# Performance work log

Measured on AMD Instinct MI355X. Metric: run time of the kernel, lower is better.

The kernel has to match this reference:

```python
import jax, jax.numpy as jnp
from jax import lax
import numpy as np

V, E, H, L, B, ML, T = 32000, 512, 512, 2, 64, 64, 32


def setup_inputs() -> dict:
    key = jax.random.key(0)
    ks = jax.random.split(key, 16)
    s = 0.05
    return {
        "current_input": jax.random.randint(ks[0], (B,), 0, V),
        "h0": jax.random.normal(ks[1], (L, B, H), jnp.float32),
        "c0": jax.random.normal(ks[2], (L, B, H), jnp.float32),
        "encoder_output": jax.random.normal(ks[3], (ML, B, H), jnp.float32),
        "gtruth": jax.random.randint(ks[4], (T, B), 0, V),
        "length": T,
        "emb": s * jax.random.normal(ks[5], (V, E), jnp.float32),
        "attn_W": s * jax.random.normal(ks[6], (ML, E + H), jnp.float32),
        "attn_out_W": s * jax.random.normal(ks[7], (E, E + H), jnp.float32),
        "lstm_Wi": s * jax.random.normal(ks[8], (L, 4 * H, E), jnp.float32),
        "lstm_Wh": s * jax.random.normal(ks[9], (L, 4 * H, H), jnp.float32),
        "lstm_bi": s * jax.random.normal(ks[10], (L, 4 * H), jnp.float32),
        "lstm_bh": s * jax.random.normal(ks[11], (L, 4 * H), jnp.float32),
        "gen_W": s * jax.random.normal(ks[12], (V, H), jnp.float32),
        "gen_b": s * jax.random.normal(ks[13], (V,), jnp.float32),
    }


def _lstm_cell(x, h, c, Wi, Wh, bi, bh):
    # PyTorch gate order: i, f, g, o
    g = x @ Wi.T + h @ Wh.T + bi + bh  # [B, 4H]
    i, f, gg, o = jnp.split(g, 4, axis=-1)
    c_new = jax.nn.sigmoid(f) * c + jax.nn.sigmoid(i) * jnp.tanh(gg)
    h_new = jax.nn.sigmoid(o) * jnp.tanh(c_new)
    return h_new, c_new


def reference(current_input, h0, c0, encoder_output, gtruth, length,
              emb, attn_W, attn_out_W, lstm_Wi, lstm_Wh, lstm_bi, lstm_bh,
              gen_W, gen_b):
    n_layers = h0.shape[0]

    def step_fn(carry, tok):
        h, c = carry  # each [L, B, H]
        emb_t = emb[tok]                                   # [B, E]
        attn_in = jnp.concatenate([emb_t, h[-1]], axis=1)  # [B, E+H]
        a = jax.nn.softmax(attn_in @ attn_W.T, axis=1)     # [B, ML]
        ctx = jnp.einsum('bl,lbh->bh', a, encoder_output)  # [B, H]
        rnn_in = jax.nn.relu(
            jnp.concatenate([emb_t, ctx], axis=1) @ attn_out_W.T)  # [B, E]
        x = rnn_in
        hs, cs = [], []
        for l in range(n_layers):
            hn, cn = _lstm_cell(x, h[l], c[l], lstm_Wi[l], lstm_Wh[l],
                                lstm_bi[l], lstm_bh[l])
            hs.append(hn)
            cs.append(cn)
            x = hn
        scores = x @ gen_W.T + gen_b  # [B, V]
        return (jnp.stack(hs), jnp.stack(cs)), scores

    # teacher forcing: step t consumes current_input at t=0, gtruth[t-1] after
    tokens = jnp.concatenate([current_input[None], gtruth[:-1]], axis=0)  # [T, B]
    (h_fin, c_fin), outputs = lax.scan(step_fn, (h0, c0), tokens)
    return outputs, h_fin, c_fin
```

## Files before the change

### kernel.cpp

```cpp
#include <hip/hip_runtime.h>
#include <hip/hip_bf16.h>

typedef __bf16 bf16_t;
typedef bf16_t bf16x8 __attribute__((ext_vector_type(8)));
typedef bf16_t bf16x4 __attribute__((ext_vector_type(4)));
typedef float f32x4 __attribute__((ext_vector_type(4)));

#define MFMA(a, b, c) __builtin_amdgcn_mfma_f32_16x16x32_bf16((a), (b), (c), 0, 0, 0)

__device__ __forceinline__ float sigm(float x) { return 1.f / (1.f + __expf(-x)); }
__device__ __forceinline__ float tanh_f(float x) { return 1.f - 2.f / (__expf(2.f * x) + 1.f); }

__device__ __forceinline__ bf16x8 cvt8(const float* p) {
    f32x4 a = *(const f32x4*)p, b = *(const f32x4*)(p + 4);
    bf16x8 v;
#pragma unroll
    for (int i = 0; i < 4; ++i) { v[i] = (bf16_t)a[i]; v[4 + i] = (bf16_t)b[i]; }
    return v;
}

__device__ __forceinline__ void st4c(bf16_t* p, bf16x4 v) {
    __hip_atomic_store((unsigned long long*)p, __builtin_bit_cast(unsigned long long, v),
                       __ATOMIC_RELAXED, __HIP_MEMORY_SCOPE_AGENT);
}
__device__ __forceinline__ void st1c(bf16_t* p, bf16_t v) {
    __hip_atomic_store((unsigned short*)p, __builtin_bit_cast(unsigned short, v),
                       __ATOMIC_RELAXED, __HIP_MEMORY_SCOPE_AGENT);
}

__device__ __forceinline__ void gbar(int* cnt, int target) {
    __syncthreads();
    if (threadIdx.x == 0) {
        __hip_atomic_fetch_add(cnt, 1, __ATOMIC_RELAXED, __HIP_MEMORY_SCOPE_AGENT);
        while (__hip_atomic_load(cnt, __ATOMIC_RELAXED, __HIP_MEMORY_SCOPE_AGENT) < target)
            __builtin_amdgcn_s_sleep(2);
    }
    __syncthreads();
}

__global__ void k_cvt(const float* __restrict__ src, bf16_t* __restrict__ dst, int n) {
    int i = (blockIdx.x * 256 + threadIdx.x) * 8;
    if (i < n) *(bf16x8*)(dst + i) = cvt8(src + i);
}

__global__ void k_init(const float* __restrict__ h0, const float* __restrict__ c0,
                       const float* __restrict__ bi, const float* __restrict__ bh,
                       float* __restrict__ c_f32, bf16_t* __restrict__ h1_0,
                       bf16_t* __restrict__ h2_0, float* __restrict__ bsum,
                       int* __restrict__ bar) {
    int idx = blockIdx.x * 256 + threadIdx.x;
    if (idx < 65536) c_f32[idx] = c0[idx];
    if (idx < 32768) { h1_0[idx] = (bf16_t)h0[idx]; h2_0[idx] = (bf16_t)h0[32768 + idx]; }
    if (idx < 4096) bsum[idx] = bi[idx] + bh[idx];
    if (idx == 0) *bar = 0;
}

__global__ __launch_bounds__(256) void k_pre(const float* __restrict__ emb,
                                             const int* __restrict__ cur, const int* __restrict__ gt,
                                             const bf16_t* __restrict__ Bm, int ldb, int koff,
                                             float* __restrict__ out, int ldo) {
    int tid = threadIdx.x, lane = tid & 63, w = tid >> 6;
    int m = lane & 15, q = lane >> 4;
    int mrow = blockIdx.x * 64 + w * 16 + m;
    int tok = (mrow < 64) ? cur[mrow] : gt[mrow - 64];
    const float* arow = emb + (size_t)tok * 512;
    int n0 = blockIdx.y * 64;
    const bf16_t* brow0 = Bm + (size_t)(n0 + m) * ldb + koff;
    f32x4 acc[4] = {};
    for (int ks = 0; ks < 16; ++ks) {
        int kc = ks * 32 + q * 8;
        bf16x8 a = cvt8(arow + kc);
#pragma unroll
        for (int nt = 0; nt < 4; ++nt) {
            bf16x8 b = *(const bf16x8*)(brow0 + (size_t)nt * 16 * ldb + kc);
            acc[nt] = MFMA(a, b, acc[nt]);
        }
    }
    int rbase = blockIdx.x * 64 + w * 16 + q * 4;
#pragma unroll
    for (int nt = 0; nt < 4; ++nt)
#pragma unroll
        for (int i = 0; i < 4; ++i)
            out[(size_t)(rbase + i) * ldo + n0 + nt * 16 + m] = acc[nt][i];
}

__device__ __forceinline__ void lstm_phase(int wg, int tid,
                                           const bf16_t* __restrict__ x,
                                           const bf16_t* __restrict__ hprev,
                                           const bf16_t* __restrict__ Wi,
                                           const bf16_t* __restrict__ Wh,
                                           const float* __restrict__ bsum,
                                           float* __restrict__ c,
                                           bf16_t* __restrict__ hout,
                                           bf16_t* __restrict__ xs_out) {
    int lane = tid & 63, w = tid >> 6;
    int m = lane & 15, q = lane >> 4;
    int j0 = wg * 16;
    const bf16_t* ax = x + (size_t)(w * 16 + m) * 512;
    const bf16_t* ah = hprev + (size_t)(w * 16 + m) * 512;
    f32x4 acc[4] = {};
    for (int ks = 0; ks < 16; ++ks) {
        int kc = ks * 32 + q * 8;
        bf16x8 a = *(const bf16x8*)(ax + kc);
#pragma unroll
        for (int g = 0; g < 4; ++g) {
            const bf16_t* bp = Wi + (size_t)(g * 512 + j0 + m) * 512 + kc;
            acc[g] = MFMA(a, *(const bf16x8*)bp, acc[g]);
        }
    }
    for (int ks = 0; ks < 16; ++ks) {
        int kc = ks * 32 + q * 8;
        bf16x8 a = *(const bf16x8*)(ah + kc);
#pragma unroll
        for (int g = 0; g < 4; ++g) {
            const bf16_t* bp = Wh + (size_t)(g * 512 + j0 + m) * 512 + kc;
            acc[g] = MFMA(a, *(const bf16x8*)bp, acc[g]);
        }
    }
    int j = j0 + m;
    float bs0 = bsum[j], bs1 = bsum[512 + j], bs2 = bsum[1024 + j], bs3 = bsum[1536 + j];
#pragma unroll
    for (int i = 0; i < 4; ++i) {
        int b = w * 16 + q * 4 + i;
        float ig = acc[0][i] + bs0;
        float fg = acc[1][i] + bs1;
        float gg = acc[2][i] + bs2;
        float og = acc[3][i] + bs3;
        size_t off = (size_t)b * 512 + j;
        float co = c[off];
        float cn = sigm(fg) * co + sigm(ig) * tanh_f(gg);
        float hn = sigm(og) * tanh_f(cn);
        c[off] = cn;
        st1c(hout + off, (bf16_t)hn);
        if (xs_out) xs_out[off] = (bf16_t)hn;
    }
}

__global__ __launch_bounds__(256) void k_loop(const bf16_t* __restrict__ attn_W_bf,
                                              const bf16_t* __restrict__ attn_out_W_bf,
                                              const float* __restrict__ enc,
                                              const float* __restrict__ pre_s,
                                              const float* __restrict__ pre_r,
                                              const bf16_t* __restrict__ Wi_bf,
                                              const bf16_t* __restrict__ Wh_bf,
                                              const float* __restrict__ bsum,
                                              float* __restrict__ c_f32,
                                              bf16_t* __restrict__ h1_buf,
                                              bf16_t* __restrict__ h2_buf,
                                              bf16_t* __restrict__ ctx_buf,
                                              bf16_t* __restrict__ rnn_buf,
                                              bf16_t* __restrict__ xs,
                                              int* __restrict__ bar) {
    __shared__ float s_p[2][64];
    int tid = threadIdx.x, lane = tid & 63, w = tid >> 6;
    int m = lane & 15, q = lane >> 4;
    int wg = blockIdx.x;
    int b0 = wg * 2;
    int bt = 0;

    for (int t = 0; t < 32; ++t) {
        const bf16_t* h1p = h1_buf + (size_t)t * 32768;
        const bf16_t* h2p = h2_buf + (size_t)t * 32768;
        bf16_t* h1n = h1_buf + (size_t)(t + 1) * 32768;
        bf16_t* h2n = h2_buf + (size_t)(t + 1) * 32768;
        bf16_t* ctx_t = ctx_buf + (size_t)t * 32768;
        const bf16_t* rnn_t = rnn_buf + (size_t)t * 32768;

        {
            const bf16_t* aptr = h2p + (size_t)(b0 + (m & 1)) * 512;
            const bf16_t* bptr = attn_W_bf + (size_t)(w * 16 + m) * 1024 + 512;
            f32x4 acc = {};
            for (int ks = 0; ks < 16; ++ks) {
                int kc = ks * 32 + q * 8;
                acc = MFMA(*(const bf16x8*)(aptr + kc), *(const bf16x8*)(bptr + kc), acc);
            }
            if (q == 0) {
#pragma unroll
                for (int i = 0; i < 2; ++i)
                    s_p[i][w * 16 + m] =
                        acc[i] + pre_s[((size_t)t * 64 + b0 + i) * 64 + w * 16 + m];
            }
        }
        __syncthreads();
        if (tid < 128) {
            int r = tid >> 6, l = tid & 63;
            float v = s_p[r][l];
            float mx = v;
#pragma unroll
            for (int off = 32; off; off >>= 1) mx = fmaxf(mx, __shfl_xor(mx, off));
            float e = __expf(v - mx);
            float s = e;
#pragma unroll
            for (int off = 32; off; off >>= 1) s += __shfl_xor(s, off);
            s_p[r][l] = e / s;
        }
        __syncthreads();
        {
            int r = tid >> 7, c0 = (tid & 127) * 4;
            int b = b0 + r;
            f32x4 acc = {};
            const float* ebase = enc + (size_t)b * 512 + c0;
            for (int l = 0; l < 64; ++l) {
                float a = s_p[r][l];
                f32x4 e = *(const f32x4*)(ebase + (size_t)l * 32768);
#pragma unroll
                for (int i = 0; i < 4; ++i) acc[i] += a * e[i];
            }
            bf16x4 cv;
#pragma unroll
            for (int i = 0; i < 4; ++i) cv[i] = (bf16_t)acc[i];
            st4c(ctx_t + (size_t)b * 512 + c0, cv);
        }
        bt += 32; gbar(bar, bt);

        {
            int j0 = wg * 16;
            const bf16_t* actx = ctx_t + (size_t)(w * 16 + m) * 512;
            const bf16_t* bptr = attn_out_W_bf + (size_t)(j0 + m) * 1024 + 512;
            f32x4 acc = {};
            for (int ks = 0; ks < 16; ++ks) {
                int kc = ks * 32 + q * 8;
                acc = MFMA(*(const bf16x8*)(actx + kc), *(const bf16x8*)(bptr + kc), acc);
            }
            int jj = j0 + m;
#pragma unroll
            for (int i = 0; i < 4; ++i) {
                int b = w * 16 + q * 4 + i;
                float v = acc[i] + pre_r[((size_t)t * 64 + b) * 512 + jj];
                st1c((bf16_t*)rnn_t + (size_t)b * 512 + jj, (bf16_t)fmaxf(v, 0.f));
            }
        }
        bt += 32; gbar(bar, bt);

        lstm_phase(wg, tid, rnn_t, h1p, Wi_bf, Wh_bf, bsum, c_f32, h1n, nullptr);
        bt += 32; gbar(bar, bt);

        lstm_phase(wg, tid, h1n, h2p, Wi_bf + 1048576, Wh_bf + 1048576, bsum + 2048,
                   c_f32 + 32768, h2n, xs + (size_t)t * 32768);
        bt += 32; gbar(bar, bt);
    }
}

__global__ __launch_bounds__(256) void k_gen(const bf16_t* __restrict__ xs,
                                             const bf16_t* __restrict__ gen_W,
                                             const float* __restrict__ gen_b,
                                             float* __restrict__ out) {
    __shared__ bf16_t sA[64 * 256];
    int tid = threadIdx.x, lane = tid & 63, w = tid >> 6;
    int m = lane & 15, q4 = lane >> 4;
    int m0 = blockIdx.x * 64, n0 = blockIdx.y * 256;
    f32x4 acc[4][4] = {};
    for (int ko = 0; ko < 2; ++ko) {
        __syncthreads();
#pragma unroll
        for (int it = 0; it < 8; ++it) {
            int idx = it * 256 + tid;
            int mr = idx >> 5, qc = idx & 31;
            bf16x8 v = *(const bf16x8*)(xs + (size_t)(m0 + mr) * 512 + ko * 256 + qc * 8);
            *(bf16x8*)(&sA[(mr * 32 + (qc ^ (mr & 7))) * 8]) = v;
        }
        __syncthreads();
        const bf16_t* bbase = gen_W + (size_t)(n0 + w * 64 + m) * 512 + ko * 256;
        for (int ks = 0; ks < 8; ++ks) {
            bf16x8 af[4];
#pragma unroll
            for (int mt = 0; mt < 4; ++mt) {
                int r = mt * 16 + m, chunk = ks * 4 + q4;
                af[mt] = *(const bf16x8*)(&sA[(r * 32 + (chunk ^ (r & 7))) * 8]);
            }
            int kc = ks * 32 + q4 * 8;
#pragma unroll
            for (int nt = 0; nt < 4; ++nt) {
                bf16x8 bfrag = *(const bf16x8*)(bbase + (size_t)nt * 16 * 512 + kc);
#pragma unroll
                for (int mt = 0; mt < 4; ++mt) acc[mt][nt] = MFMA(af[mt], bfrag, acc[mt][nt]);
            }
        }
    }
#pragma unroll
    for (int nt = 0; nt < 4; ++nt) {
        int col = n0 + w * 64 + nt * 16 + m;
        float bias = gen_b[col];
#pragma unroll
        for (int mt = 0; mt < 4; ++mt)
#pragma unroll
            for (int i = 0; i < 4; ++i) {
                int r = m0 + mt * 16 + q4 * 4 + i;
                out[(size_t)r * 32000 + col] = acc[mt][nt][i] + bias;
            }
    }
}

__global__ void k_tail(const bf16_t* __restrict__ h1f, const bf16_t* __restrict__ h2f,
                       const float* __restrict__ c_f32, float* __restrict__ out) {
    int idx = blockIdx.x * 256 + threadIdx.x;
    if (idx < 65536) {
        float hv = (idx < 32768) ? (float)h1f[idx] : (float)h2f[idx - 32768];
        out[65536000 + idx] = hv;
        out[65601536 + idx] = c_f32[idx];
    }
}

extern "C" void kernel_launch(void* const* d_in, const int* in_sizes, int n_in,
                              void* d_out, int out_size, void* d_ws, size_t ws_size,
                              hipStream_t stream) {
    const int* cur = (const int*)d_in[0];
    const float* h0 = (const float*)d_in[1];
    const float* c0 = (const float*)d_in[2];
    const float* enc = (const float*)d_in[3];
    const int* gt = (const int*)d_in[4];
    const float* emb = (const float*)d_in[6];
    const float* attn_W = (const float*)d_in[7];
    const float* attn_out_W = (const float*)d_in[8];
    const float* Wi = (const float*)d_in[9];
    const float* Wh = (const float*)d_in[10];
    const float* bi = (const float*)d_in[11];
    const float* bh = (const float*)d_in[12];
    const float* gen_W = (const float*)d_in[13];
    const float* gen_b = (const float*)d_in[14];
    float* out = (float*)d_out;

    char* ws = (char*)d_ws;
    float* c_f32 = (float*)(ws + 0);
    float* bsum = (float*)(ws + 524288);
    float* pre_s = (float*)(ws + 540672);
    float* pre_r = (float*)(ws + 1064960);
    bf16_t* xs = (bf16_t*)(ws + 5324800);
    bf16_t* attn_W_bf = (bf16_t*)(ws + 7421952);
    bf16_t* attn_out_W_bf = (bf16_t*)(ws + 7553024);
    bf16_t* Wi_bf = (bf16_t*)(ws + 8601600);
    bf16_t* Wh_bf = (bf16_t*)(ws + 12795904);
    bf16_t* gen_W_bf = (bf16_t*)(ws + 16990208);
    bf16_t* h1_buf = (bf16_t*)(ws + 49758208);
    bf16_t* h2_buf = (bf16_t*)(ws + 51920896);
    bf16_t* ctx_buf = (bf16_t*)(ws + 54083584);
    bf16_t* rnn_buf = (bf16_t*)(ws + 56180736);
    int* bar = (int*)(ws + 58277888);

    k_cvt<<<32, 256, 0, stream>>>(attn_W, attn_W_bf, 65536);
    k_cvt<<<256, 256, 0, stream>>>(attn_out_W, attn_out_W_bf, 524288);
    k_cvt<<<1024, 256, 0, stream>>>(Wi, Wi_bf, 2097152);
    k_cvt<<<1024, 256, 0, stream>>>(Wh, Wh_bf, 2097152);
    k_cvt<<<8000, 256, 0, stream>>>(gen_W, gen_W_bf, 16384000);
    k_init<<<256, 256, 0, stream>>>(h0, c0, bi, bh, c_f32, h1_buf, h2_buf, bsum, bar);
    k_pre<<<dim3(32, 1), 256, 0, stream>>>(emb, cur, gt, attn_W_bf, 1024, 0, pre_s, 64);
    k_pre<<<dim3(32, 8), 256, 0, stream>>>(emb, cur, gt, attn_out_W_bf, 1024, 0, pre_r, 512);

    k_loop<<<32, 256, 0, stream>>>(attn_W_bf, attn_out_W_bf, enc, pre_s, pre_r,
                                   Wi_bf, Wh_bf, bsum, c_f32, h1_buf, h2_buf,
                                   ctx_buf, rnn_buf, xs, bar);

    k_gen<<<dim3(32, 125), 256, 0, stream>>>(xs, gen_W_bf, gen_b, out);
    k_tail<<<256, 256, 0, stream>>>(h1_buf + 32 * 32768, h2_buf + 32 * 32768, c_f32, out);
}
```

Measured before the change: 3.574 ms.

## Keep attention context in LDS and replace counter barrier with per-block flags

Each workgroup now computes the attention output projection for its own two batch rows straight from a shared-memory copy of the context, instead of publishing the context to global memory and waiting on a grid barrier. This removes one of the four grid-wide barriers per step, at the cost of each block reading the full attn_out weight slice, which is redundant across blocks. The grid barrier is also reimplemented as per-block epoch flags on padded cache lines, polled by 32 lanes, replacing a single contended atomic counter. The MFMA tile now wastes 14 of its 16 rows because only two batch rows are real.

```diff
diff --git a/kernel.cpp b/kernel.cpp
--- a/kernel.cpp
+++ b/kernel.cpp
@@ -19,21 +19,20 @@
     return v;
 }
 
-__device__ __forceinline__ void st4c(bf16_t* p, bf16x4 v) {
-    __hip_atomic_store((unsigned long long*)p, __builtin_bit_cast(unsigned long long, v),
-                       __ATOMIC_RELAXED, __HIP_MEMORY_SCOPE_AGENT);
-}
 __device__ __forceinline__ void st1c(bf16_t* p, bf16_t v) {
     __hip_atomic_store((unsigned short*)p, __builtin_bit_cast(unsigned short, v),
                        __ATOMIC_RELAXED, __HIP_MEMORY_SCOPE_AGENT);
 }
 
-__device__ __forceinline__ void gbar(int* cnt, int target) {
+__device__ __forceinline__ void gbar(int* flags, int wg, int epoch) {
     __syncthreads();
-    if (threadIdx.x == 0) {
-        __hip_atomic_fetch_add(cnt, 1, __ATOMIC_RELAXED, __HIP_MEMORY_SCOPE_AGENT);
-        while (__hip_atomic_load(cnt, __ATOMIC_RELAXED, __HIP_MEMORY_SCOPE_AGENT) < target)
-            __builtin_amdgcn_s_sleep(2);
+    if (threadIdx.x < 64) {
+        if (threadIdx.x == 0)
+            __hip_atomic_store(flags + wg * 16, epoch, __ATOMIC_RELAXED,
+                               __HIP_MEMORY_SCOPE_AGENT);
+        int* f = flags + (threadIdx.x & 31) * 16;
+        while (__hip_atomic_load(f, __ATOMIC_RELAXED, __HIP_MEMORY_SCOPE_AGENT) < epoch)
+            __builtin_amdgcn_s_sleep(1);
     }
     __syncthreads();
 }
@@ -47,12 +46,12 @@
                        const float* __restrict__ bi, const float* __restrict__ bh,
                        float* __restrict__ c_f32, bf16_t* __restrict__ h1_0,
                        bf16_t* __restrict__ h2_0, float* __restrict__ bsum,
-                       int* __restrict__ bar) {
+                       int* __restrict__ flags) {
     int idx = blockIdx.x * 256 + threadIdx.x;
     if (idx < 65536) c_f32[idx] = c0[idx];
     if (idx < 32768) { h1_0[idx] = (bf16_t)h0[idx]; h2_0[idx] = (bf16_t)h0[32768 + idx]; }
     if (idx < 4096) bsum[idx] = bi[idx] + bh[idx];
-    if (idx == 0) *bar = 0;
+    if (idx < 512) flags[idx] = 0;
 }
 
 __global__ __launch_bounds__(256) void k_pre(const float* __restrict__ emb,
@@ -147,24 +146,23 @@
                                               float* __restrict__ c_f32,
                                               bf16_t* __restrict__ h1_buf,
                                               bf16_t* __restrict__ h2_buf,
-                                              bf16_t* __restrict__ ctx_buf,
                                               bf16_t* __restrict__ rnn_buf,
                                               bf16_t* __restrict__ xs,
-                                              int* __restrict__ bar) {
+                                              int* __restrict__ flags) {
     __shared__ float s_p[2][64];
+    __shared__ bf16_t s_ctx[2][512];
     int tid = threadIdx.x, lane = tid & 63, w = tid >> 6;
     int m = lane & 15, q = lane >> 4;
     int wg = blockIdx.x;
     int b0 = wg * 2;
-    int bt = 0;
+    int ep = 0;
 
     for (int t = 0; t < 32; ++t) {
         const bf16_t* h1p = h1_buf + (size_t)t * 32768;
         const bf16_t* h2p = h2_buf + (size_t)t * 32768;
         bf16_t* h1n = h1_buf + (size_t)(t + 1) * 32768;
         bf16_t* h2n = h2_buf + (size_t)(t + 1) * 32768;
-        bf16_t* ctx_t = ctx_buf + (size_t)t * 32768;
-        const bf16_t* rnn_t = rnn_buf + (size_t)t * 32768;
+        bf16_t* rnn_t = rnn_buf + (size_t)t * 32768;
 
         {
             const bf16_t* aptr = h2p + (size_t)(b0 + (m & 1)) * 512;
@@ -209,35 +207,42 @@
             bf16x4 cv;
 #pragma unroll
             for (int i = 0; i < 4; ++i) cv[i] = (bf16_t)acc[i];
-            st4c(ctx_t + (size_t)b * 512 + c0, cv);
-        }
-        bt += 32; gbar(bar, bt);
-
+            *(bf16x4*)(&s_ctx[r][c0]) = cv;
+        }
+        __syncthreads();
         {
-            int j0 = wg * 16;
-            const bf16_t* actx = ctx_t + (size_t)(w * 16 + m) * 512;
-            const bf16_t* bptr = attn_out_W_bf + (size_t)(j0 + m) * 1024 + 512;
-            f32x4 acc = {};
+            const bf16_t* actx = &s_ctx[m & 1][0];
+            const bf16_t* bbase = attn_out_W_bf + (size_t)(w * 128 + m) * 1024 + 512;
+            f32x4 acc[8] = {};
             for (int ks = 0; ks < 16; ++ks) {
                 int kc = ks * 32 + q * 8;
-                acc = MFMA(*(const bf16x8*)(actx + kc), *(const bf16x8*)(bptr + kc), acc);
-            }
-            int jj = j0 + m;
-#pragma unroll
-            for (int i = 0; i < 4; ++i) {
-                int b = w * 16 + q * 4 + i;
-                float v = acc[i] + pre_r[((size_t)t * 64 + b) * 512 + jj];
-                st1c((bf16_t*)rnn_t + (size_t)b * 512 + jj, (bf16_t)fmaxf(v, 0.f));
-            }
-        }
-        bt += 32; gbar(bar, bt);
+                bf16x8 a = *(const bf16x8*)(actx + kc);
+#pragma unroll
+                for (int nt = 0; nt < 8; ++nt) {
+                    bf16x8 b = *(const bf16x8*)(bbase + (size_t)nt * 16 * 1024 + kc);
+                    acc[nt] = MFMA(a, b, acc[nt]);
+                }
+            }
+#pragma unroll
+            for (int nt = 0; nt < 8; ++nt)
+#pragma unroll
+                for (int i = 0; i < 4; ++i) {
+                    int r = q * 4 + i;
+                    if (r < 2) {
+                        int b = b0 + r, jj = w * 128 + nt * 16 + m;
+                        float v = acc[nt][i] + pre_r[((size_t)t * 64 + b) * 512 + jj];
+                        st1c(rnn_t + (size_t)b * 512 + jj, (bf16_t)fmaxf(v, 0.f));
+                    }
+                }
+        }
+        gbar(flags, wg, ++ep);
 
         lstm_phase(wg, tid, rnn_t, h1p, Wi_bf, Wh_bf, bsum, c_f32, h1n, nullptr);
-        bt += 32; gbar(bar, bt);
+        gbar(flags, wg, ++ep);
 
         lstm_phase(wg, tid, h1n, h2p, Wi_bf + 1048576, Wh_bf + 1048576, bsum + 2048,
                    c_f32 + 32768, h2n, xs + (size_t)t * 32768);
-        bt += 32; gbar(bar, bt);
+        gbar(flags, wg, ++ep);
     }
 }
 
@@ -333,22 +338,21 @@
     bf16_t* gen_W_bf = (bf16_t*)(ws + 16990208);
     bf16_t* h1_buf = (bf16_t*)(ws + 49758208);
     bf16_t* h2_buf = (bf16_t*)(ws + 51920896);
-    bf16_t* ctx_buf = (bf16_t*)(ws + 54083584);
-    bf16_t* rnn_buf = (bf16_t*)(ws + 56180736);
-    int* bar = (int*)(ws + 58277888);
+    bf16_t* rnn_buf = (bf16_t*)(ws + 54083584);
+    int* flags = (int*)(ws + 56180736);
 
     k_cvt<<<32, 256, 0, stream>>>(attn_W, attn_W_bf, 65536);
     k_cvt<<<256, 256, 0, stream>>>(attn_out_W, attn_out_W_bf, 524288);
     k_cvt<<<1024, 256, 0, stream>>>(Wi, Wi_bf, 2097152);
     k_cvt<<<1024, 256, 0, stream>>>(Wh, Wh_bf, 2097152);
     k_cvt<<<8000, 256, 0, stream>>>(gen_W, gen_W_bf, 16384000);
-    k_init<<<256, 256, 0, stream>>>(h0, c0, bi, bh, c_f32, h1_buf, h2_buf, bsum, bar);
+    k_init<<<256, 256, 0, stream>>>(h0, c0, bi, bh, c_f32, h1_buf, h2_buf, bsum, flags);
     k_pre<<<dim3(32, 1), 256, 0, stream>>>(emb, cur, gt, attn_W_bf, 1024, 0, pre_s, 64);
     k_pre<<<dim3(32, 8), 256, 0, stream>>>(emb, cur, gt, attn_out_W_bf, 1024, 0, pre_r, 512);
 
     k_loop<<<32, 256, 0, stream>>>(attn_W_bf, attn_out_W_bf, enc, pre_s, pre_r,
                                    Wi_bf, Wh_bf, bsum, c_f32, h1_buf, h2_buf,
-                                   ctx_buf, rnn_buf, xs, bar);
+                                   rnn_buf, xs, flags);
 
     k_gen<<<dim3(32, 125), 256, 0, stream>>>(xs, gen_W_bf, gen_b, out);
     k_tail<<<256, 256, 0, stream>>>(h1_buf + 32 * 32768, h2_buf + 32 * 32768, c_f32, out);
```

Measured after the change: 4.535 ms. 1.27x slower.
